# Optimization experiments

Hardware: AMD Instinct MI355X
Metric: run time of the kernel (lower is better)

Reference implementation:

```python
import jax, jax.numpy as jnp
import numpy as np

N = 32768; NS = 16; C_MAIN = 128; C_MOD = 128; C_IN = 16; SHARE = 8
EPS = 1e-5; CHUNK = 1024
C_OUT = C_MAIN + C_MOD  # out_main = in_main + in_mod
C_W = C_IN // SHARE     # attention-weight channels = 2


def _bn(x, g, b, m, v):
    # BatchNorm1d in eval mode, per last-dim channel
    return (x - m) / jnp.sqrt(v + EPS) * g + b


def _knn(p, k):
    # exact kNN (self included, distance 0), chunked to bound memory
    def f(q):  # q: (CHUNK, 3)
        d = jnp.sum((q[:, None, :] - p[None, :, :]) ** 2, axis=-1)  # (CHUNK, N)
        return jax.lax.top_k(-d, k)[1]
    return jax.lax.map(f, p.reshape(-1, CHUNK, 3)).reshape(-1, k)


def setup_inputs() -> dict:
    key = jax.random.key(0)
    ks = iter(jax.random.split(key, 24))
    rn = lambda shape, s=0.1: jax.random.normal(next(ks), shape, jnp.float32) * s
    inp = {}
    inp["x_main"] = jax.random.normal(next(ks), (N, C_MAIN), jnp.float32)
    inp["x_mod"] = jax.random.normal(next(ks), (N, C_MOD), jnp.float32)
    inp["xyz"] = jax.random.uniform(next(ks), (N, 3), dtype=jnp.float32)
    inp["W_ein"] = rn((C_OUT, C_IN)); inp["b_ein"] = rn((C_IN,))
    inp["W_eout"] = rn((C_IN, C_OUT)); inp["b_eout"] = rn((C_OUT,))
    inp["Wq"] = rn((C_IN, C_IN)); inp["bq"] = rn((C_IN,))
    inp["Wk"] = rn((C_IN, C_IN)); inp["bk"] = rn((C_IN,))
    inp["Wv"] = rn((C_IN, C_IN)); inp["bv"] = rn((C_IN,))
    inp["Wp1"] = rn((3, 3)); inp["bp1"] = rn((3,))
    inp["Wp2"] = rn((3, C_IN)); inp["bp2"] = rn((C_IN,))
    inp["Wl1"] = rn((C_IN, C_W)); inp["bl1"] = rn((C_W,))
    inp["Wl2"] = rn((C_W, C_W)); inp["bl2"] = rn((C_W,))
    for name, c in (("bn_p", 3), ("bn_w1", C_IN), ("bn_w2", C_W)):
        inp[name + "_g"] = jnp.ones(c, jnp.float32)
        inp[name + "_b"] = jnp.zeros(c, jnp.float32)
        inp[name + "_m"] = jnp.zeros(c, jnp.float32)
        inp[name + "_v"] = jnp.ones(c, jnp.float32)
    return inp


def _forward(x_main, x_mod, xyz, W_ein, b_ein, W_eout, b_eout, Wq, bq, Wk, bk, Wv, bv,
             Wp1, bp1, Wp2, bp2, Wl1, bl1, Wl2, bl2,
             bn_p_g, bn_p_b, bn_p_m, bn_p_v,
             bn_w1_g, bn_w1_b, bn_w1_m, bn_w1_v,
             bn_w2_g, bn_w2_b, bn_w2_m, bn_w2_v, idx):
    x_fused = jnp.concatenate([x_main, x_mod], axis=-1)   # (N, 256)
    x_res = x_fused
    h = x_fused @ W_ein + b_ein                           # E_in: (N, 16)
    # PointTransformerLayer (local vector self-attention over NS neighbors)
    xq = h @ Wq + bq
    xk = h @ Wk + bk
    xv = h @ Wv + bv
    p_r = xyz[idx] - xyz[:, None, :]                      # relative coords (N, NS, 3)
    g_k = xk[idx]                                         # grouped keys   (N, NS, 16)
    g_v = xv[idx]                                         # grouped values (N, NS, 16)
    # linear_p: Linear(3,3) -> BN -> ReLU -> Linear(3, C_IN)
    t = jax.nn.relu(_bn(p_r @ Wp1 + bp1, bn_p_g, bn_p_b, bn_p_m, bn_p_v))
    p_e = t @ Wp2 + bp2                                   # (N, NS, 16)
    # out_planes//mid_planes == 1, so the .view(...).sum(2) on p_e is identity
    w = g_k - xq[:, None, :] + p_e
    # linear_w: BN -> ReLU -> Linear(16,2) -> BN -> ReLU -> Linear(2,2)
    w = jax.nn.relu(_bn(w, bn_w1_g, bn_w1_b, bn_w1_m, bn_w1_v))
    w = w @ Wl1 + bl1
    w = jax.nn.relu(_bn(w, bn_w2_g, bn_w2_b, bn_w2_m, bn_w2_v))
    w = w @ Wl2 + bl2                                     # (N, NS, 2)
    w = jax.nn.softmax(w, axis=1)                         # softmax over neighbors
    agg = ((g_v + p_e).reshape(N, NS, SHARE, C_W) * w[:, :, None, :]).sum(1).reshape(N, C_IN)
    return agg @ W_eout + b_eout + x_res                  # E_out + residual


def reference(x_main, x_mod, xyz, W_ein, b_ein, W_eout, b_eout, Wq, bq, Wk, bk, Wv, bv,
              Wp1, bp1, Wp2, bp2, Wl1, bl1, Wl2, bl2,
              bn_p_g, bn_p_b, bn_p_m, bn_p_v,
              bn_w1_g, bn_w1_b, bn_w1_m, bn_w1_v,
              bn_w2_g, bn_w2_b, bn_w2_m, bn_w2_v):
    idx = _knn(xyz, NS)
    return _forward(x_main, x_mod, xyz, W_ein, b_ein, W_eout, b_eout, Wq, bq, Wk, bk, Wv, bv,
                    Wp1, bp1, Wp2, bp2, Wl1, bl1, Wl2, bl2,
                    bn_p_g, bn_p_b, bn_p_m, bn_p_v,
                    bn_w1_g, bn_w1_b, bn_w1_m, bn_w1_v,
                    bn_w2_g, bn_w2_b, bn_w2_m, bn_w2_v, idx)
```

## Files before the change

### kernel.cpp

```cpp
#include <hip/hip_runtime.h>
#include <cstdint>

#define NPTS 32768
#define K 16
#define G 16
#define NCELL (G*G*G)

typedef unsigned short u16;
typedef unsigned int u32;
typedef unsigned long long u64;

__device__ __forceinline__ float bf(u16 v) { return __uint_as_float(((u32)v) << 16); }
__device__ __forceinline__ void unp(u32 u, float& a, float& b) {
    a = __uint_as_float(u << 16);
    b = __uint_as_float(u & 0xffff0000u);
}
__device__ __forceinline__ u32 f2b(float f) {
    u32 x = __float_as_uint(f);
    return (x + 0x7fffu + ((x >> 16) & 1u)) >> 16;
}
__device__ __forceinline__ float ldw(const void* p, int j, bool isb) {
    return isb ? bf(((const u16*)p)[j]) : ((const float*)p)[j];
}
__device__ __forceinline__ void ld8(const void* p, size_t i, int cb, bool isb, float xs[8]) {
    if (isb) {
        const uint4* r = (const uint4*)((const u16*)p + i * 128);
        const uint4 u = r[cb];
        unp(u.x, xs[0], xs[1]); unp(u.y, xs[2], xs[3]);
        unp(u.z, xs[4], xs[5]); unp(u.w, xs[6], xs[7]);
    } else {
        const float4* r = (const float4*)((const float*)p + i * 128);
        const float4 a = r[2 * cb], b = r[2 * cb + 1];
        xs[0] = a.x; xs[1] = a.y; xs[2] = a.z; xs[3] = a.w;
        xs[4] = b.x; xs[5] = b.y; xs[6] = b.z; xs[7] = b.w;
    }
}
__device__ __forceinline__ int cellco(float x) {
    int c = (int)(x * (float)G);
    return c < 0 ? 0 : (c > G - 1 ? G - 1 : c);
}
__device__ __forceinline__ u64 shflx64(u64 v, int m) {
    return (u64)__shfl_xor((long long)v, m, 64);
}
__device__ __forceinline__ float dist_np(float4 q, float4 c) {
    const float dx = __fsub_rn(q.x, c.x);
    const float dy = __fsub_rn(q.y, c.y);
    const float dz = __fsub_rn(q.z, c.z);
    return __fadd_rn(__fadd_rn(__fmul_rn(dx, dx), __fmul_rn(dy, dy)), __fmul_rn(dz, dz));
}
__device__ __forceinline__ u64 key64(float d, int idx) {
    return ((u64)__float_as_uint(d) << 32) | (u32)idx;
}

__global__ __launch_bounds__(256) void k_feats(
    const void* __restrict__ xm, const void* __restrict__ xd, const void* __restrict__ xyz,
    const void* __restrict__ Wein, const void* __restrict__ bein,
    const void* __restrict__ Wq, const void* __restrict__ bq,
    const void* __restrict__ Wk, const void* __restrict__ bk,
    const void* __restrict__ Wv, const void* __restrict__ bv,
    const u32* __restrict__ sigp,
    float* __restrict__ oq, float* __restrict__ ok, float* __restrict__ ov,
    float4* __restrict__ xyzf, int* __restrict__ cellCnt,
    int* __restrict__ ptCell, int* __restrict__ ptRank)
{
    const bool isb = (*sigp == 0x3F803F80u);
    __shared__ float sW[4096];
    __shared__ float sM[768];
    __shared__ float sB[64];
    const int t = threadIdx.x;
    for (int u = t; u < 4096; u += 256) sW[u] = ldw(Wein, u, isb);
    if (t < 256) { sM[t] = ldw(Wq, t, isb); sM[256 + t] = ldw(Wk, t, isb); sM[512 + t] = ldw(Wv, t, isb); }
    if (t < 64) {
        const void* bsrc = (t < 16) ? bein : (t < 32) ? bq : (t < 48) ? bk : bv;
        sB[t] = ldw(bsrc, t & 15, isb);
    }
    __syncthreads();
    const int r = blockIdx.x * 128 + (t >> 1);
    const int half = t & 1;
    float hp[16];
#pragma unroll
    for (int j = 0; j < 16; ++j) hp[j] = half ? 0.f : sB[j];
    const void* src = half ? xd : xm;
    const int wbase = half * 128;
#pragma unroll 2
    for (int cb = 0; cb < 16; ++cb) {
        float xs[8];
        ld8(src, (size_t)r, cb, isb, xs);
#pragma unroll
        for (int u = 0; u < 8; ++u) {
            const float x = xs[u];
            const float* w = &sW[(wbase + cb * 8 + u) * 16];
#pragma unroll
            for (int j = 0; j < 16; ++j) hp[j] = fmaf(x, w[j], hp[j]);
        }
    }
    float h[16];
#pragma unroll
    for (int j = 0; j < 16; ++j) h[j] = hp[j] + __shfl_xor(hp[j], 1, 64);
    const float* wm = half ? &sM[256] : &sM[0];
    const float* bm = half ? &sB[32] : &sB[16];
    float acc[16];
#pragma unroll
    for (int j = 0; j < 16; ++j) acc[j] = bm[j];
#pragma unroll
    for (int m = 0; m < 16; ++m) {
        const float hm = h[m];
#pragma unroll
        for (int j = 0; j < 16; ++j) acc[j] = fmaf(hm, wm[m * 16 + j], acc[j]);
    }
    float4* o4 = (float4*)((half ? ok : oq) + (size_t)r * 16);
#pragma unroll
    for (int j4 = 0; j4 < 4; ++j4)
        o4[j4] = make_float4(acc[4 * j4], acc[4 * j4 + 1], acc[4 * j4 + 2], acc[4 * j4 + 3]);
    float vacc[8];
    const int vo = half * 8;
#pragma unroll
    for (int u = 0; u < 8; ++u) vacc[u] = sB[48 + vo + u];
#pragma unroll
    for (int m = 0; m < 16; ++m) {
        const float hm = h[m];
#pragma unroll
        for (int u = 0; u < 8; ++u) vacc[u] = fmaf(hm, sM[512 + m * 16 + vo + u], vacc[u]);
    }
    float4* v4 = (float4*)(ov + (size_t)r * 16 + vo);
    v4[0] = make_float4(vacc[0], vacc[1], vacc[2], vacc[3]);
    v4[1] = make_float4(vacc[4], vacc[5], vacc[6], vacc[7]);
    if (half == 0) {
        float px, py, pz;
        if (isb) { const u16* z = (const u16*)xyz; px = bf(z[r * 3]); py = bf(z[r * 3 + 1]); pz = bf(z[r * 3 + 2]); }
        else { const float* z = (const float*)xyz; px = z[r * 3]; py = z[r * 3 + 1]; pz = z[r * 3 + 2]; }
        xyzf[r] = make_float4(px, py, pz, 0.f);
        const int c = (cellco(pz) * G + cellco(py)) * G + cellco(px);
        ptCell[r] = c;
        ptRank[r] = atomicAdd(&cellCnt[c], 1);
    }
}

__global__ __launch_bounds__(256) void k_scatter(const float4* __restrict__ xyzf,
    const int* __restrict__ ptCell, const int* __restrict__ ptRank,
    const int* __restrict__ cellCnt, int* __restrict__ starts, float4* __restrict__ sorted)
{
    __shared__ int sSt[NCELL];
    __shared__ int wsum[4];
    const int t = threadIdx.x;
    int c[16];
    {
        const int4* cc = (const int4*)cellCnt;
#pragma unroll
        for (int u = 0; u < 4; ++u) {
            const int4 v = cc[t * 4 + u];
            c[4 * u] = v.x; c[4 * u + 1] = v.y; c[4 * u + 2] = v.z; c[4 * u + 3] = v.w;
        }
    }
    int s = 0;
#pragma unroll
    for (int u = 0; u < 16; ++u) s += c[u];
    int inc = s;
#pragma unroll
    for (int off = 1; off < 64; off <<= 1) {
        const int v = __shfl_up(inc, off, 64);
        if ((t & 63) >= off) inc += v;
    }
    if ((t & 63) == 63) wsum[t >> 6] = inc;
    __syncthreads();
    int pre = 0;
    for (int w = 0; w < (t >> 6); ++w) pre += wsum[w];
    int run = pre + inc - s;
#pragma unroll
    for (int u = 0; u < 16; ++u) { sSt[t * 16 + u] = run; run += c[u]; }
    __syncthreads();
    const int i = blockIdx.x * 256 + t;
    float4 p = xyzf[i];
    p.w = __int_as_float(i);
    sorted[sSt[ptCell[i]] + ptRank[i]] = p;
    if (blockIdx.x == 0) {
#pragma unroll
        for (int u = 0; u < 16; ++u) starts[t * 16 + u] = sSt[t * 16 + u];
        if (t == 0) starts[NCELL] = NPTS;
    }
}

__device__ __forceinline__ void ins16(u64 kb, u64 key[K]) {
    if (kb < key[K - 1]) {
#pragma unroll
        for (int j = 0; j < K; ++j) {
            const bool lt = kb < key[j];
            const u64 tk = lt ? key[j] : kb;
            key[j] = lt ? kb : key[j];
            kb = tk;
        }
    }
}
__device__ __forceinline__ void merge16k(u64 k[K], int mask) {
    u64 pk[K];
#pragma unroll
    for (int i = 0; i < K; ++i) pk[i] = shflx64(k[K - 1 - i], mask);
#pragma unroll
    for (int i = 0; i < K; ++i) k[i] = k[i] < pk[i] ? k[i] : pk[i];
#pragma unroll
    for (int ks = 8; ks >= 1; ks >>= 1) {
#pragma unroll
        for (int i = 0; i < K; ++i) {
            if ((i & ks) == 0) {
                const int j = i + ks;
                const u64 a = k[i], b = k[j];
                k[i] = a < b ? a : b;
                k[j] = a < b ? b : a;
            }
        }
    }
}
__device__ __forceinline__ float guard_radius(float qx, float qy, float qz,
                                              int cx, int cy, int cz, int R)
{
    const float h = 1.0f / (float)G;
    float rg = 3.4e38f;
    if (cx - R >= 1)     rg = fminf(rg, qx - (float)(cx - R) * h);
    if (cx + R <= G - 2) rg = fminf(rg, (float)(cx + R + 1) * h - qx);
    if (cy - R >= 1)     rg = fminf(rg, qy - (float)(cy - R) * h);
    if (cy + R <= G - 2) rg = fminf(rg, (float)(cy + R + 1) * h - qy);
    if (cz - R >= 1)     rg = fminf(rg, qz - (float)(cz - R) * h);
    if (cz + R <= G - 2) rg = fminf(rg, (float)(cz + R + 1) * h - qz);
    return rg;
}
__device__ __forceinline__ void scan_run8(const float4* __restrict__ sorted,
    int b, int e, int l, float4 me, u64 tk, u64 key[K])
{
    int p = b + l;
    if (p >= e) return;
    float4 c = sorted[p];
    while (true) {
        const int pn = p + 8;
        const bool more = pn < e;
        float4 cnx = c;
        if (more) cnx = sorted[pn];
        const u64 kb = key64(dist_np(me, c), __float_as_int(c.w));
        if (kb <= tk) ins16(kb, key);
        if (!more) break;
        c = cnx; p = pn;
    }
}

__global__ __launch_bounds__(256) void k_knng(const float4* __restrict__ sorted,
    const int* __restrict__ starts, int* __restrict__ idxOut)
{
    const int g = blockIdx.x * 256 + threadIdx.x;
    const int s = g >> 3;
    const int l = g & 7;
    const float4 me = sorted[s];
    const int cx = cellco(me.x), cy = cellco(me.y), cz = cellco(me.z);
    const float h = 1.0f / (float)G;

    int rb[9]; int rc[10]; rc[0] = 0;
    {
        const int x0 = cx - 1 < 0 ? 0 : cx - 1;
        const int x1 = cx + 1 > G - 1 ? G - 1 : cx + 1;
#pragma unroll
        for (int r = 0; r < 9; ++r) {
            const int dz = r / 3 - 1, dy = r % 3 - 1;
            const int zz = cz + dz, yy = cy + dy;
            int b = 0, len = 0;
            if ((unsigned)zz <= (unsigned)(G - 1) && (unsigned)yy <= (unsigned)(G - 1)) {
                const int base = (zz * G + yy) * G;
                b = starts[base + x0];
                len = starts[base + x1 + 1] - b;
            }
            rb[r] = b;
            rc[r + 1] = rc[r] + len;
        }
    }
    const int tot = rc[9];
    int bias[9];
#pragma unroll
    for (int r = 0; r < 9; ++r) bias[r] = rb[r] - rc[r];

#define FLAT(f) ({ int _b = bias[0]; \
    _Pragma("unroll") for (int _r = 1; _r < 9; ++_r) _b = ((f) >= rc[_r]) ? bias[_r] : _b; \
    (f) + _b; })

    u64 kA0 = ~0ull, kA1 = ~0ull;
    {
        int p0 = l, p1 = l + 8, p2 = l + 16, p3 = l + 24;
        float4 c0 = sorted[p0 < tot ? FLAT(p0) : 0];
        float4 c1 = sorted[p1 < tot ? FLAT(p1) : 0];
        float4 c2 = sorted[p2 < tot ? FLAT(p2) : 0];
        float4 c3 = sorted[p3 < tot ? FLAT(p3) : 0];
        while (p0 < tot) {
            const int q0 = p0 + 32, q1 = p1 + 32, q2 = p2 + 32, q3 = p3 + 32;
            float4 n0 = sorted[q0 < tot ? FLAT(q0) : 0];
            float4 n1 = sorted[q1 < tot ? FLAT(q1) : 0];
            float4 n2 = sorted[q2 < tot ? FLAT(q2) : 0];
            float4 n3 = sorted[q3 < tot ? FLAT(q3) : 0];
            u64 kb;
#define TOP2(c, valid) \
            kb = (valid) ? key64(dist_np(me, c), __float_as_int((c).w)) : ~0ull; \
            { const bool c0lt = kb < kA0, c1lt = kb < kA1; \
              const u64 nk1 = c0lt ? kA0 : kb; \
              kA1 = c1lt ? nk1 : kA1; \
              kA0 = c0lt ? kb : kA0; }
            TOP2(c0, true);
            TOP2(c1, p1 < tot);
            TOP2(c2, p2 < tot);
            TOP2(c3, p3 < tot);
#undef TOP2
            p0 = q0; p1 = q1; p2 = q2; p3 = q3;
            c0 = n0; c1 = n1; c2 = n2; c3 = n3;
        }
    }
    u64 tau0 = kA1;
#pragma unroll
    for (int m = 1; m <= 4; m <<= 1) { const u64 o = shflx64(tau0, m); tau0 = o > tau0 ? o : tau0; }

    u64 key[K];
#pragma unroll
    for (int j = 0; j < K; ++j) key[j] = ~0ull;
    {
        int p0 = l, p1 = l + 8, p2 = l + 16, p3 = l + 24;
        float4 c0 = sorted[p0 < tot ? FLAT(p0) : 0];
        float4 c1 = sorted[p1 < tot ? FLAT(p1) : 0];
        float4 c2 = sorted[p2 < tot ? FLAT(p2) : 0];
        float4 c3 = sorted[p3 < tot ? FLAT(p3) : 0];
        while (p0 < tot) {
            const int q0 = p0 + 32, q1 = p1 + 32, q2 = p2 + 32, q3 = p3 + 32;
            float4 n0 = sorted[q0 < tot ? FLAT(q0) : 0];
            float4 n1 = sorted[q1 < tot ? FLAT(q1) : 0];
            float4 n2 = sorted[q2 < tot ? FLAT(q2) : 0];
            float4 n3 = sorted[q3 < tot ? FLAT(q3) : 0];
            u64 kb;
#define INSF(c, valid) \
            kb = key64(dist_np(me, c), __float_as_int((c).w)); \
            if ((valid) && kb <= tau0) ins16(kb, key);
            INSF(c0, true);
            INSF(c1, p1 < tot);
            INSF(c2, p2 < tot);
            INSF(c3, p3 < tot);
#undef INSF
            p0 = q0; p1 = q1; p2 = q2; p3 = q3;
            c0 = n0; c1 = n1; c2 = n2; c3 = n3;
        }
    }
#undef FLAT

    merge16k(key, 1); merge16k(key, 2); merge16k(key, 4);

    int R = 1;
    while (R < G) {
        const u64 tk = key[K - 1];
        const float rg = guard_radius(me.x, me.y, me.z, cx, cy, cz, R);
        if (tk < ((u64)__float_as_uint(rg * rg * 0.9999f) << 32)) break;
        if (l != 0) {
#pragma unroll
            for (int j = 0; j < K; ++j) key[j] = ~0ull;
        }
        ++R;
        for (int dz = -R; dz <= R; ++dz) {
            const int zz = cz + dz;
            if ((unsigned)zz > (unsigned)(G - 1)) continue;
            const int az = dz < 0 ? -dz : dz;
            const float dzd = dz < 0 ? me.z - (float)(cz + dz + 1) * h : dz > 0 ? (float)(cz + dz) * h - me.z : 0.f;
            for (int dy = -R; dy <= R; ++dy) {
                const int yy = cy + dy;
                if ((unsigned)yy > (unsigned)(G - 1)) continue;
                const int ay = dy < 0 ? -dy : dy;
                const float dyd = dy < 0 ? me.y - (float)(cy + dy + 1) * h : dy > 0 ? (float)(cy + dy) * h - me.y : 0.f;
                const float myz = dzd * dzd + dyd * dyd;
                const int base = (zz * G + yy) * G;
                if (az == R || ay == R) {
                    if (tk < ((u64)__float_as_uint(myz * 0.9999f) << 32)) continue;
                    const int x0 = cx - R < 0 ? 0 : cx - R;
                    const int x1 = cx + R > G - 1 ? G - 1 : cx + R;
                    scan_run8(sorted, starts[base + x0], starts[base + x1 + 1], l, me, tk, key);
                } else {
                    if (cx - R >= 0) {
                        const float xd = me.x - (float)(cx - R + 1) * h;
                        if (!(tk < ((u64)__float_as_uint((myz + xd * xd) * 0.9999f) << 32)))
                            scan_run8(sorted, starts[base + cx - R], starts[base + cx - R + 1], l, me, tk, key);
                    }
                    if (cx + R <= G - 1) {
                        const float xd = (float)(cx + R) * h - me.x;
                        if (!(tk < ((u64)__float_as_uint((myz + xd * xd) * 0.9999f) << 32)))
                            scan_run8(sorted, starts[base + cx + R], starts[base + cx + R + 1], l, me, tk, key);
                    }
                }
            }
        }
        merge16k(key, 1); merge16k(key, 2); merge16k(key, 4);
    }
    if (l == 0) {
        const int orig = __float_as_int(me.w);
        int4* o = (int4*)(idxOut + (size_t)orig * K);
#pragma unroll
        for (int j4 = 0; j4 < 4; ++j4)
            o[j4] = make_int4((int)(u32)key[4 * j4], (int)(u32)key[4 * j4 + 1],
                              (int)(u32)key[4 * j4 + 2], (int)(u32)key[4 * j4 + 3]);
    }
}

__global__ __launch_bounds__(256) void k_attn(
    const void* __restrict__ xm, const void* __restrict__ xd,
    const float4* __restrict__ xyzf,
    const float* __restrict__ xq, const float* __restrict__ xk, const float* __restrict__ xv,
    const int* __restrict__ idx,
    const void* __restrict__ Weout, const void* __restrict__ beout,
    const void* __restrict__ Wp1, const void* __restrict__ bp1,
    const void* __restrict__ Wp2, const void* __restrict__ bp2,
    const void* __restrict__ Wl1, const void* __restrict__ bl1,
    const void* __restrict__ Wl2, const void* __restrict__ bl2,
    const void* __restrict__ bnp_g, const void* __restrict__ bnp_b, const void* __restrict__ bnp_m, const void* __restrict__ bnp_v,
    const void* __restrict__ bw1_g, const void* __restrict__ bw1_b, const void* __restrict__ bw1_m, const void* __restrict__ bw1_v,
    const void* __restrict__ bw2_g, const void* __restrict__ bw2_b, const void* __restrict__ bw2_m, const void* __restrict__ bw2_v,
    void* __restrict__ out)
{
    const bool isb = (*(const u32*)bnp_g == 0x3F803F80u);
    __shared__ float sWe[4096];
    __shared__ float sbe[256];
    __shared__ float sWp2[48];
    __shared__ float sbp2[16];
    __shared__ float sWl1[32];
    __shared__ float s1[16], o1[16];
    const int t = threadIdx.x;
    for (int u = t; u < 4096; u += 256) sWe[u] = ldw(Weout, u, isb);
    if (t < 256) sbe[t] = ldw(beout, t, isb);
    if (t < 48) sWp2[t] = ldw(Wp2, t, isb);
    if (t < 16) sbp2[t] = ldw(bp2, t, isb);
    if (t < 32) sWl1[t] = ldw(Wl1, t, isb);
    if (t < 16) {
        const float s = ldw(bw1_g, t, isb) / sqrtf(ldw(bw1_v, t, isb) + 1e-5f);
        s1[t] = s; o1[t] = ldw(bw1_b, t, isb) - ldw(bw1_m, t, isb) * s;
    }
    __syncthreads();
    const int g = blockIdx.x * 256 + t;
    const int s = g >> 3;
    const int l = g & 7;
    float Wp1r[9], bp1r[3], sp[3], op[3];
#pragma unroll
    for (int u = 0; u < 9; ++u) Wp1r[u] = ldw(Wp1, u, isb);
#pragma unroll
    for (int a = 0; a < 3; ++a) {
        const float sc = ldw(bnp_g, a, isb) / sqrtf(ldw(bnp_v, a, isb) + 1e-5f);
        sp[a] = sc; op[a] = ldw(bnp_b, a, isb) - ldw(bnp_m, a, isb) * sc;
        bp1r[a] = ldw(bp1, a, isb);
    }
    float Wl2r[4], bl1r[2], bl2r[2], s2[2], o2[2];
#pragma unroll
    for (int u = 0; u < 4; ++u) Wl2r[u] = ldw(Wl2, u, isb);
#pragma unroll
    for (int c = 0; c < 2; ++c) {
        bl1r[c] = ldw(bl1, c, isb); bl2r[c] = ldw(bl2, c, isb);
        const float sc = ldw(bw2_g, c, isb) / sqrtf(ldw(bw2_v, c, isb) + 1e-5f);
        s2[c] = sc; o2[c] = ldw(bw2_b, c, isb) - ldw(bw2_m, c, isb) * sc;
    }
    float q[16];
    const float4* qrow = (const float4*)(xq + (size_t)s * 16);
#pragma unroll
    for (int j4 = 0; j4 < 4; ++j4) {
        const float4 v = qrow[j4];
        q[4 * j4] = v.x; q[4 * j4 + 1] = v.y; q[4 * j4 + 2] = v.z; q[4 * j4 + 3] = v.w;
    }
    const int2 nb2 = ((const int2*)(idx + (size_t)s * 16))[l];
    const int nb[2] = { nb2.x, nb2.y };
    const float4 cp = xyzf[s];
    float wa[2], wb[2], ttx[2], tty[2], ttz[2];
#pragma unroll
    for (int n = 0; n < 2; ++n) {
        const int nn = nb[n];
        const float4 pp = xyzf[nn];
        const float prx = pp.x - cp.x, pry = pp.y - cp.y, prz = pp.z - cp.z;
        float tt[3];
#pragma unroll
        for (int a = 0; a < 3; ++a) {
            float v = prx * Wp1r[a] + pry * Wp1r[3 + a] + prz * Wp1r[6 + a] + bp1r[a];
            v = fmaf(v, sp[a], op[a]);
            tt[a] = v > 0.f ? v : 0.f;
        }
        ttx[n] = tt[0]; tty[n] = tt[1]; ttz[n] = tt[2];
        const float4* k4 = (const float4*)(xk + (size_t)nn * 16);
        float kk[16];
#pragma unroll
        for (int j4 = 0; j4 < 4; ++j4) {
            const float4 v = k4[j4];
            kk[4 * j4] = v.x; kk[4 * j4 + 1] = v.y; kk[4 * j4 + 2] = v.z; kk[4 * j4 + 3] = v.w;
        }
        float wl0 = bl1r[0], wl1v = bl1r[1];
#pragma unroll
        for (int j = 0; j < 16; ++j) {
            const float pe = tt[0] * sWp2[j] + tt[1] * sWp2[16 + j] + tt[2] * sWp2[32 + j] + sbp2[j];
            float w = kk[j] - q[j] + pe;
            w = fmaf(w, s1[j], o1[j]); w = w > 0.f ? w : 0.f;
            wl0 = fmaf(w, sWl1[2 * j], wl0);
            wl1v = fmaf(w, sWl1[2 * j + 1], wl1v);
        }
        float y0 = fmaf(wl0, s2[0], o2[0]); y0 = y0 > 0.f ? y0 : 0.f;
        float y1 = fmaf(wl1v, s2[1], o2[1]); y1 = y1 > 0.f ? y1 : 0.f;
        wa[n] = y0 * Wl2r[0] + y1 * Wl2r[2] + bl2r[0];
        wb[n] = y0 * Wl2r[1] + y1 * Wl2r[3] + bl2r[1];
    }
    float m0 = fmaxf(wa[0], wa[1]), m1 = fmaxf(wb[0], wb[1]);
#pragma unroll
    for (int m = 1; m <= 4; m <<= 1) {
        m0 = fmaxf(m0, __shfl_xor(m0, m, 64));
        m1 = fmaxf(m1, __shfl_xor(m1, m, 64));
    }
    float sA = 0.f, sB = 0.f;
#pragma unroll
    for (int n = 0; n < 2; ++n) {
        wa[n] = __expf(wa[n] - m0); sA += wa[n];
        wb[n] = __expf(wb[n] - m1); sB += wb[n];
    }
#pragma unroll
    for (int m = 1; m <= 4; m <<= 1) {
        sA += __shfl_xor(sA, m, 64);
        sB += __shfl_xor(sB, m, 64);
    }
    const float rA = 1.f / sA, rB = 1.f / sB;
    float agg[16];
#pragma unroll
    for (int j = 0; j < 16; ++j) agg[j] = 0.f;
#pragma unroll
    for (int n = 0; n < 2; ++n) {
        const float wA = wa[n] * rA, wB = wb[n] * rB;
        const float4* v4 = (const float4*)(xv + (size_t)nb[n] * 16);
        float vv[16];
#pragma unroll
        for (int j4 = 0; j4 < 4; ++j4) {
            const float4 v = v4[j4];
            vv[4 * j4] = v.x; vv[4 * j4 + 1] = v.y; vv[4 * j4 + 2] = v.z; vv[4 * j4 + 3] = v.w;
        }
#pragma unroll
        for (int j = 0; j < 16; ++j) {
            const float pe = ttx[n] * sWp2[j] + tty[n] * sWp2[16 + j] + ttz[n] * sWp2[32 + j] + sbp2[j];
            agg[j] = fmaf(vv[j] + pe, (j & 1) ? wB : wA, agg[j]);
        }
    }
#pragma unroll
    for (int j = 0; j < 16; ++j) {
        agg[j] += __shfl_xor(agg[j], 1, 64);
        agg[j] += __shfl_xor(agg[j], 2, 64);
        agg[j] += __shfl_xor(agg[j], 4, 64);
    }
#pragma unroll 1
    for (int obi = 0; obi < 4; ++obi) {
        const int ob = obi * 8 + l;
        float xs[8];
        ld8((ob < 16) ? xm : xd, (size_t)s, ob & 15, isb, xs);
        const int o0 = ob * 8;
        float acc[8];
#pragma unroll
        for (int u = 0; u < 8; ++u) acc[u] = sbe[o0 + u] + xs[u];
#pragma unroll
        for (int j = 0; j < 16; ++j) {
            const float aj = agg[j];
            const float* w = &sWe[j * 256 + o0];
#pragma unroll
            for (int u = 0; u < 8; ++u) acc[u] = fmaf(aj, w[u], acc[u]);
        }
        if (isb) {
            u32* orow = (u32*)out + (size_t)s * 128;
#pragma unroll
            for (int u = 0; u < 4; ++u)
                orow[ob * 4 + u] = f2b(acc[2 * u]) | (f2b(acc[2 * u + 1]) << 16);
        } else {
            float4* orow = (float4*)((float*)out + (size_t)s * 256);
            orow[2 * ob]     = make_float4(acc[0], acc[1], acc[2], acc[3]);
            orow[2 * ob + 1] = make_float4(acc[4], acc[5], acc[6], acc[7]);
        }
    }
}

extern "C" void kernel_launch(void* const* d_in, const int* in_sizes, int n_in,
                              void* d_out, int out_size, void* d_ws, size_t ws_size,
                              hipStream_t stream)
{
    (void)in_sizes; (void)n_in; (void)out_size; (void)ws_size;
    const void* xm   = d_in[0];
    const void* xd   = d_in[1];
    const void* xyz  = d_in[2];
    const void* Wein = d_in[3];
    const void* bein = d_in[4];
    const void* Weout= d_in[5];
    const void* beout= d_in[6];
    const void* Wq   = d_in[7];
    const void* bq   = d_in[8];
    const void* Wk   = d_in[9];
    const void* bk   = d_in[10];
    const void* Wv   = d_in[11];
    const void* bv   = d_in[12];
    const void* Wp1  = d_in[13];
    const void* bp1  = d_in[14];
    const void* Wp2  = d_in[15];
    const void* bp2  = d_in[16];
    const void* Wl1  = d_in[17];
    const void* bl1  = d_in[18];
    const void* Wl2  = d_in[19];
    const void* bl2  = d_in[20];
    const void* bnp_g = d_in[21];
    const void* bnp_b = d_in[22];
    const void* bnp_m = d_in[23];
    const void* bnp_v = d_in[24];
    const void* bw1_g = d_in[25];
    const void* bw1_b = d_in[26];
    const void* bw1_m = d_in[27];
    const void* bw1_v = d_in[28];
    const void* bw2_g = d_in[29];
    const void* bw2_b = d_in[30];
    const void* bw2_m = d_in[31];
    const void* bw2_v = d_in[32];

    char* ws = (char*)d_ws;
    const size_t MB = 1024 * 1024;
    float*  oq    = (float*)(ws);
    float*  ok    = (float*)(ws + 2 * MB);
    float*  ov    = (float*)(ws + 4 * MB);
    int*    idx   = (int*)  (ws + 6 * MB);
    float4* xyzf  = (float4*)(ws + 8 * MB);
    float4* sortp = (float4*)(ws + 8 * MB + 512 * 1024);
    int* cellCnt  = (int*)(ws + 9 * MB);
    int* starts   = (int*)(ws + 9 * MB + 32 * 1024);
    int* ptCell   = (int*)(ws + 9 * MB + 64 * 1024);
    int* ptRank   = (int*)(ws + 9 * MB + 192 * 1024);

    hipMemsetAsync(cellCnt, 0, NCELL * sizeof(int), stream);
    k_feats<<<dim3(NPTS * 2 / 256), dim3(256), 0, stream>>>(
        xm, xd, xyz, Wein, bein, Wq, bq, Wk, bk, Wv, bv,
        (const u32*)bnp_g, oq, ok, ov, xyzf, cellCnt, ptCell, ptRank);
    k_scatter<<<dim3(NPTS / 256), dim3(256), 0, stream>>>(xyzf, ptCell, ptRank, cellCnt, starts, sortp);
    k_knng<<<dim3(NPTS * 8 / 256), dim3(256), 0, stream>>>(sortp, starts, idx);
    k_attn<<<dim3(NPTS * 8 / 256), dim3(256), 0, stream>>>(
        xm, xd, xyzf, oq, ok, ov, idx, Weout, beout, Wp1, bp1, Wp2, bp2,
        Wl1, bl1, Wl2, bl2, bnp_g, bnp_b, bnp_m, bnp_v,
        bw1_g, bw1_b, bw1_m, bw1_v, bw2_g, bw2_b, bw2_m, bw2_v, d_out);
}
```

Measured before the change: 258.4 us.

## Store K/V in bf16 and map one thread per neighbor in attention kernel

```diff
diff --git a/kernel.cpp b/kernel.cpp
--- a/kernel.cpp
+++ b/kernel.cpp
@@ -19,6 +19,7 @@
     u32 x = __float_as_uint(f);
     return (x + 0x7fffu + ((x >> 16) & 1u)) >> 16;
 }
+__device__ __forceinline__ u32 pk2(float a, float b) { return f2b(a) | (f2b(b) << 16); }
 __device__ __forceinline__ float ldw(const void* p, int j, bool isb) {
     return isb ? bf(((const u16*)p)[j]) : ((const float*)p)[j];
 }
@@ -59,7 +60,7 @@
     const void* __restrict__ Wk, const void* __restrict__ bk,
     const void* __restrict__ Wv, const void* __restrict__ bv,
     const u32* __restrict__ sigp,
-    float* __restrict__ oq, float* __restrict__ ok, float* __restrict__ ov,
+    float* __restrict__ oq, u32* __restrict__ okb, u32* __restrict__ ovb,
     float4* __restrict__ xyzf, int* __restrict__ cellCnt,
     int* __restrict__ ptCell, int* __restrict__ ptRank)
 {
@@ -108,10 +109,16 @@
 #pragma unroll
         for (int j = 0; j < 16; ++j) acc[j] = fmaf(hm, wm[m * 16 + j], acc[j]);
     }
-    float4* o4 = (float4*)((half ? ok : oq) + (size_t)r * 16);
-#pragma unroll
-    for (int j4 = 0; j4 < 4; ++j4)
-        o4[j4] = make_float4(acc[4 * j4], acc[4 * j4 + 1], acc[4 * j4 + 2], acc[4 * j4 + 3]);
+    if (half == 0) {
+        float4* o4 = (float4*)(oq + (size_t)r * 16);
+#pragma unroll
+        for (int j4 = 0; j4 < 4; ++j4)
+            o4[j4] = make_float4(acc[4 * j4], acc[4 * j4 + 1], acc[4 * j4 + 2], acc[4 * j4 + 3]);
+    } else {
+        uint4* kr = (uint4*)(okb + (size_t)r * 8);
+        kr[0] = make_uint4(pk2(acc[0], acc[1]), pk2(acc[2], acc[3]), pk2(acc[4], acc[5]), pk2(acc[6], acc[7]));
+        kr[1] = make_uint4(pk2(acc[8], acc[9]), pk2(acc[10], acc[11]), pk2(acc[12], acc[13]), pk2(acc[14], acc[15]));
+    }
     float vacc[8];
     const int vo = half * 8;
 #pragma unroll
@@ -122,9 +129,8 @@
 #pragma unroll
         for (int u = 0; u < 8; ++u) vacc[u] = fmaf(hm, sM[512 + m * 16 + vo + u], vacc[u]);
     }
-    float4* v4 = (float4*)(ov + (size_t)r * 16 + vo);
-    v4[0] = make_float4(vacc[0], vacc[1], vacc[2], vacc[3]);
-    v4[1] = make_float4(vacc[4], vacc[5], vacc[6], vacc[7]);
+    uint4* vr = (uint4*)(ovb + (size_t)r * 8 + half * 4);
+    *vr = make_uint4(pk2(vacc[0], vacc[1]), pk2(vacc[2], vacc[3]), pk2(vacc[4], vacc[5]), pk2(vacc[6], vacc[7]));
     if (half == 0) {
         float px, py, pz;
         if (isb) { const u16* z = (const u16*)xyz; px = bf(z[r * 3]); py = bf(z[r * 3 + 1]); pz = bf(z[r * 3 + 2]); }
@@ -399,7 +405,7 @@
 __global__ __launch_bounds__(256) void k_attn(
     const void* __restrict__ xm, const void* __restrict__ xd,
     const float4* __restrict__ xyzf,
-    const float* __restrict__ xq, const float* __restrict__ xk, const float* __restrict__ xv,
+    const float* __restrict__ xq, const u32* __restrict__ kb, const u32* __restrict__ vb,
     const int* __restrict__ idx,
     const void* __restrict__ Weout, const void* __restrict__ beout,
     const void* __restrict__ Wp1, const void* __restrict__ bp1,
@@ -430,8 +436,33 @@
     }
     __syncthreads();
     const int g = blockIdx.x * 256 + t;
-    const int s = g >> 3;
-    const int l = g & 7;
+    const int s = g >> 4;
+    const int l = g & 15;
+
+    const int nn = idx[(size_t)s * 16 + l];
+    const uint4* kr = (const uint4*)(kb + (size_t)nn * 8);
+    const uint4 k0 = kr[0], k1 = kr[1];
+    const uint4* vr = (const uint4*)(vb + (size_t)nn * 8);
+    const uint4 v0 = vr[0], v1 = vr[1];
+    const float4 pp = xyzf[nn];
+    const float4 cp = xyzf[s];
+    float q[16];
+    {
+        const float4* qrow = (const float4*)(xq + (size_t)s * 16);
+#pragma unroll
+        for (int j4 = 0; j4 < 4; ++j4) {
+            const float4 v = qrow[j4];
+            q[4 * j4] = v.x; q[4 * j4 + 1] = v.y; q[4 * j4 + 2] = v.z; q[4 * j4 + 3] = v.w;
+        }
+    }
+    float xs[16];
+    {
+        const void* src = (l < 8) ? xm : xd;
+        const int cb0 = (l & 7) * 2;
+        ld8(src, (size_t)s, cb0, isb, xs);
+        ld8(src, (size_t)s, cb0 + 1, isb, xs + 8);
+    }
+
     float Wp1r[9], bp1r[3], sp[3], op[3];
 #pragma unroll
     for (int u = 0; u < 9; ++u) Wp1r[u] = ldw(Wp1, u, isb);
@@ -450,120 +481,82 @@
         const float sc = ldw(bw2_g, c, isb) / sqrtf(ldw(bw2_v, c, isb) + 1e-5f);
         s2[c] = sc; o2[c] = ldw(bw2_b, c, isb) - ldw(bw2_m, c, isb) * sc;
     }
-    float q[16];
-    const float4* qrow = (const float4*)(xq + (size_t)s * 16);
-#pragma unroll
-    for (int j4 = 0; j4 < 4; ++j4) {
-        const float4 v = qrow[j4];
-        q[4 * j4] = v.x; q[4 * j4 + 1] = v.y; q[4 * j4 + 2] = v.z; q[4 * j4 + 3] = v.w;
-    }
-    const int2 nb2 = ((const int2*)(idx + (size_t)s * 16))[l];
-    const int nb[2] = { nb2.x, nb2.y };
-    const float4 cp = xyzf[s];
-    float wa[2], wb[2], ttx[2], tty[2], ttz[2];
-#pragma unroll
-    for (int n = 0; n < 2; ++n) {
-        const int nn = nb[n];
-        const float4 pp = xyzf[nn];
-        const float prx = pp.x - cp.x, pry = pp.y - cp.y, prz = pp.z - cp.z;
-        float tt[3];
-#pragma unroll
-        for (int a = 0; a < 3; ++a) {
-            float v = prx * Wp1r[a] + pry * Wp1r[3 + a] + prz * Wp1r[6 + a] + bp1r[a];
-            v = fmaf(v, sp[a], op[a]);
-            tt[a] = v > 0.f ? v : 0.f;
-        }
-        ttx[n] = tt[0]; tty[n] = tt[1]; ttz[n] = tt[2];
-        const float4* k4 = (const float4*)(xk + (size_t)nn * 16);
-        float kk[16];
-#pragma unroll
-        for (int j4 = 0; j4 < 4; ++j4) {
-            const float4 v = k4[j4];
-            kk[4 * j4] = v.x; kk[4 * j4 + 1] = v.y; kk[4 * j4 + 2] = v.z; kk[4 * j4 + 3] = v.w;
-        }
-        float wl0 = bl1r[0], wl1v = bl1r[1];
-#pragma unroll
-        for (int j = 0; j < 16; ++j) {
-            const float pe = tt[0] * sWp2[j] + tt[1] * sWp2[16 + j] + tt[2] * sWp2[32 + j] + sbp2[j];
-            float w = kk[j] - q[j] + pe;
-            w = fmaf(w, s1[j], o1[j]); w = w > 0.f ? w : 0.f;
-            wl0 = fmaf(w, sWl1[2 * j], wl0);
-            wl1v = fmaf(w, sWl1[2 * j + 1], wl1v);
-        }
-        float y0 = fmaf(wl0, s2[0], o2[0]); y0 = y0 > 0.f ? y0 : 0.f;
-        float y1 = fmaf(wl1v, s2[1], o2[1]); y1 = y1 > 0.f ? y1 : 0.f;
-        wa[n] = y0 * Wl2r[0] + y1 * Wl2r[2] + bl2r[0];
-        wb[n] = y0 * Wl2r[1] + y1 * Wl2r[3] + bl2r[1];
-    }
-    float m0 = fmaxf(wa[0], wa[1]), m1 = fmaxf(wb[0], wb[1]);
-#pragma unroll
-    for (int m = 1; m <= 4; m <<= 1) {
+
+    const float prx = pp.x - cp.x, pry = pp.y - cp.y, prz = pp.z - cp.z;
+    float tt[3];
+#pragma unroll
+    for (int a = 0; a < 3; ++a) {
+        float v = prx * Wp1r[a] + pry * Wp1r[3 + a] + prz * Wp1r[6 + a] + bp1r[a];
+        v = fmaf(v, sp[a], op[a]);
+        tt[a] = v > 0.f ? v : 0.f;
+    }
+    float kk[16];
+    unp(k0.x, kk[0], kk[1]); unp(k0.y, kk[2], kk[3]); unp(k0.z, kk[4], kk[5]); unp(k0.w, kk[6], kk[7]);
+    unp(k1.x, kk[8], kk[9]); unp(k1.y, kk[10], kk[11]); unp(k1.z, kk[12], kk[13]); unp(k1.w, kk[14], kk[15]);
+    float pe[16];
+    float wl0 = bl1r[0], wl1v = bl1r[1];
+#pragma unroll
+    for (int j = 0; j < 16; ++j) {
+        pe[j] = tt[0] * sWp2[j] + tt[1] * sWp2[16 + j] + tt[2] * sWp2[32 + j] + sbp2[j];
+        float w = kk[j] - q[j] + pe[j];
+        w = fmaf(w, s1[j], o1[j]); w = w > 0.f ? w : 0.f;
+        wl0 = fmaf(w, sWl1[2 * j], wl0);
+        wl1v = fmaf(w, sWl1[2 * j + 1], wl1v);
+    }
+    float y0 = fmaf(wl0, s2[0], o2[0]); y0 = y0 > 0.f ? y0 : 0.f;
+    float y1 = fmaf(wl1v, s2[1], o2[1]); y1 = y1 > 0.f ? y1 : 0.f;
+    float wa = y0 * Wl2r[0] + y1 * Wl2r[2] + bl2r[0];
+    float wb = y0 * Wl2r[1] + y1 * Wl2r[3] + bl2r[1];
+
+    float m0 = wa, m1 = wb;
+#pragma unroll
+    for (int m = 1; m <= 8; m <<= 1) {
         m0 = fmaxf(m0, __shfl_xor(m0, m, 64));
         m1 = fmaxf(m1, __shfl_xor(m1, m, 64));
     }
-    float sA = 0.f, sB = 0.f;
-#pragma unroll
-    for (int n = 0; n < 2; ++n) {
-        wa[n] = __expf(wa[n] - m0); sA += wa[n];
-        wb[n] = __expf(wb[n] - m1); sB += wb[n];
-    }
-#pragma unroll
-    for (int m = 1; m <= 4; m <<= 1) {
+    float eA = __expf(wa - m0), eB = __expf(wb - m1);
+    float sA = eA, sB = eB;
+#pragma unroll
+    for (int m = 1; m <= 8; m <<= 1) {
         sA += __shfl_xor(sA, m, 64);
         sB += __shfl_xor(sB, m, 64);
     }
-    const float rA = 1.f / sA, rB = 1.f / sB;
+    const float wA = eA / sA, wB = eB / sB;
+
+    float vv[16];
+    unp(v0.x, vv[0], vv[1]); unp(v0.y, vv[2], vv[3]); unp(v0.z, vv[4], vv[5]); unp(v0.w, vv[6], vv[7]);
+    unp(v1.x, vv[8], vv[9]); unp(v1.y, vv[10], vv[11]); unp(v1.z, vv[12], vv[13]); unp(v1.w, vv[14], vv[15]);
     float agg[16];
 #pragma unroll
-    for (int j = 0; j < 16; ++j) agg[j] = 0.f;
-#pragma unroll
-    for (int n = 0; n < 2; ++n) {
-        const float wA = wa[n] * rA, wB = wb[n] * rB;
-        const float4* v4 = (const float4*)(xv + (size_t)nb[n] * 16);
-        float vv[16];
-#pragma unroll
-        for (int j4 = 0; j4 < 4; ++j4) {
-            const float4 v = v4[j4];
-            vv[4 * j4] = v.x; vv[4 * j4 + 1] = v.y; vv[4 * j4 + 2] = v.z; vv[4 * j4 + 3] = v.w;
-        }
-#pragma unroll
-        for (int j = 0; j < 16; ++j) {
-            const float pe = ttx[n] * sWp2[j] + tty[n] * sWp2[16 + j] + ttz[n] * sWp2[32 + j] + sbp2[j];
-            agg[j] = fmaf(vv[j] + pe, (j & 1) ? wB : wA, agg[j]);
-        }
-    }
+    for (int j = 0; j < 16; ++j) agg[j] = (vv[j] + pe[j]) * ((j & 1) ? wB : wA);
 #pragma unroll
     for (int j = 0; j < 16; ++j) {
         agg[j] += __shfl_xor(agg[j], 1, 64);
         agg[j] += __shfl_xor(agg[j], 2, 64);
         agg[j] += __shfl_xor(agg[j], 4, 64);
-    }
-#pragma unroll 1
-    for (int obi = 0; obi < 4; ++obi) {
-        const int ob = obi * 8 + l;
-        float xs[8];
-        ld8((ob < 16) ? xm : xd, (size_t)s, ob & 15, isb, xs);
-        const int o0 = ob * 8;
-        float acc[8];
-#pragma unroll
-        for (int u = 0; u < 8; ++u) acc[u] = sbe[o0 + u] + xs[u];
-#pragma unroll
-        for (int j = 0; j < 16; ++j) {
-            const float aj = agg[j];
-            const float* w = &sWe[j * 256 + o0];
-#pragma unroll
-            for (int u = 0; u < 8; ++u) acc[u] = fmaf(aj, w[u], acc[u]);
-        }
-        if (isb) {
-            u32* orow = (u32*)out + (size_t)s * 128;
-#pragma unroll
-            for (int u = 0; u < 4; ++u)
-                orow[ob * 4 + u] = f2b(acc[2 * u]) | (f2b(acc[2 * u + 1]) << 16);
-        } else {
-            float4* orow = (float4*)((float*)out + (size_t)s * 256);
-            orow[2 * ob]     = make_float4(acc[0], acc[1], acc[2], acc[3]);
-            orow[2 * ob + 1] = make_float4(acc[4], acc[5], acc[6], acc[7]);
-        }
+        agg[j] += __shfl_xor(agg[j], 8, 64);
+    }
+
+    const int o0 = l * 16;
+    float acc[16];
+#pragma unroll
+    for (int u = 0; u < 16; ++u) acc[u] = sbe[o0 + u] + xs[u];
+#pragma unroll
+    for (int j = 0; j < 16; ++j) {
+        const float aj = agg[j];
+        const float* w = &sWe[j * 256 + o0];
+#pragma unroll
+        for (int u = 0; u < 16; ++u) acc[u] = fmaf(aj, w[u], acc[u]);
+    }
+    if (isb) {
+        uint4* orow = (uint4*)((u32*)out + (size_t)s * 128) + l * 2;
+        orow[0] = make_uint4(pk2(acc[0], acc[1]), pk2(acc[2], acc[3]), pk2(acc[4], acc[5]), pk2(acc[6], acc[7]));
+        orow[1] = make_uint4(pk2(acc[8], acc[9]), pk2(acc[10], acc[11]), pk2(acc[12], acc[13]), pk2(acc[14], acc[15]));
+    } else {
+        float4* orow = (float4*)((float*)out + (size_t)s * 256) + l * 4;
+#pragma unroll
+        for (int j4 = 0; j4 < 4; ++j4)
+            orow[j4] = make_float4(acc[4 * j4], acc[4 * j4 + 1], acc[4 * j4 + 2], acc[4 * j4 + 3]);
     }
 }
 
@@ -609,24 +602,24 @@
     char* ws = (char*)d_ws;
     const size_t MB = 1024 * 1024;
     float*  oq    = (float*)(ws);
-    float*  ok    = (float*)(ws + 2 * MB);
-    float*  ov    = (float*)(ws + 4 * MB);
-    int*    idx   = (int*)  (ws + 6 * MB);
-    float4* xyzf  = (float4*)(ws + 8 * MB);
-    float4* sortp = (float4*)(ws + 8 * MB + 512 * 1024);
-    int* cellCnt  = (int*)(ws + 9 * MB);
-    int* starts   = (int*)(ws + 9 * MB + 32 * 1024);
-    int* ptCell   = (int*)(ws + 9 * MB + 64 * 1024);
-    int* ptRank   = (int*)(ws + 9 * MB + 192 * 1024);
+    u32*    okb   = (u32*) (ws + 2 * MB);
+    u32*    ovb   = (u32*) (ws + 3 * MB);
+    int*    idx   = (int*) (ws + 4 * MB);
+    float4* xyzf  = (float4*)(ws + 6 * MB);
+    float4* sortp = (float4*)(ws + 6 * MB + 512 * 1024);
+    int* cellCnt  = (int*)(ws + 7 * MB);
+    int* starts   = (int*)(ws + 7 * MB + 32 * 1024);
+    int* ptCell   = (int*)(ws + 7 * MB + 64 * 1024);
+    int* ptRank   = (int*)(ws + 7 * MB + 192 * 1024);
 
     hipMemsetAsync(cellCnt, 0, NCELL * sizeof(int), stream);
     k_feats<<<dim3(NPTS * 2 / 256), dim3(256), 0, stream>>>(
         xm, xd, xyz, Wein, bein, Wq, bq, Wk, bk, Wv, bv,
-        (const u32*)bnp_g, oq, ok, ov, xyzf, cellCnt, ptCell, ptRank);
+        (const u32*)bnp_g, oq, okb, ovb, xyzf, cellCnt, ptCell, ptRank);
     k_scatter<<<dim3(NPTS / 256), dim3(256), 0, stream>>>(xyzf, ptCell, ptRank, cellCnt, starts, sortp);
     k_knng<<<dim3(NPTS * 8 / 256), dim3(256), 0, stream>>>(sortp, starts, idx);
-    k_attn<<<dim3(NPTS * 8 / 256), dim3(256), 0, stream>>>(
-        xm, xd, xyzf, oq, ok, ov, idx, Weout, beout, Wp1, bp1, Wp2, bp2,
+    k_attn<<<dim3(NPTS * 16 / 256), dim3(256), 0, stream>>>(
+        xm, xd, xyzf, oq, okb, ovb, idx, Weout, beout, Wp1, bp1, Wp2, bp2,
         Wl1, bl1, Wl2, bl2, bnp_g, bnp_b, bnp_m, bnp_v,
         bw1_g, bw1_b, bw1_m, bw1_v, bw2_g, bw2_b, bw2_m, bw2_v, d_out);
 }
```

Measured after the change: 264.5 us. 1.02x slower.
